# Performance work log

Measured on AMD Instinct MI355X. Metric: run time of the kernel, lower is better.

## Reference

```python
import jax, jax.numpy as jnp
import numpy as np

TEMPERATURE = 0.07
EPS = 1e-8
B, D, C = 4096, 512, 10


def setup_inputs() -> dict:
    key = jax.random.key(0)
    k1, k2 = jax.random.split(key)
    features = jax.random.normal(k1, (B, D), dtype=jnp.float32)
    cls = jax.random.randint(k2, (B,), 0, C)
    labels = jax.nn.one_hot(cls, C, dtype=jnp.float32)  # [B, C] one-hot
    return {"features": features, "labels": labels}


def reference(features, labels):
    b = features.shape[0]
    # L2-normalize rows
    feats = features / jnp.linalg.norm(features, axis=1, keepdims=True)
    sim = jnp.clip(feats @ feats.T / TEMPERATURE, -20.0, 20.0)  # [B, B]
    eye = jnp.eye(b, dtype=bool)
    sim = jnp.where(eye, -jnp.inf, sim)  # mask self-similarity

    labels_norm = labels / (labels.sum(axis=1, keepdims=True) + EPS)
    label_sim = labels_norm @ labels_norm.T  # [B, B]
    label_sim = jnp.where(eye, 0.0, label_sim)
    pos_mask = label_sim > 0.1  # [B, B] bool

    exp_sim = jnp.exp(sim)  # diag -> exp(-inf) = 0
    pos_sum = jnp.sum(jnp.where(pos_mask, exp_sim, 0.0), axis=1)  # [B]
    all_sum = jnp.sum(exp_sim, axis=1)  # diag already zero => off-diagonal sum
    loss_i = -jnp.log(pos_sum / (all_sum + EPS) + EPS)  # [B]

    valid = jnp.any(pos_mask, axis=1)  # rows with >=1 positive
    n_valid = jnp.sum(valid.astype(jnp.float32))
    total = jnp.sum(jnp.where(valid, loss_i, 0.0))
    return jnp.where(n_valid > 0, total / n_valid, 0.0)
```

## Files before the change

### kernel.cpp

```cpp
#include <hip/hip_runtime.h>


#define B_ROWS 4096
#define D_DIM  512
#define C_CLS  10
#define NT     64
#define NTILES (NT * (NT + 1) / 2)

typedef float f32x4 __attribute__((ext_vector_type(4)));

__device__ __forceinline__ void load_lds16(const void* g, void* l) {
  __builtin_amdgcn_global_load_lds(
      (const __attribute__((address_space(1))) unsigned int*)g,
      (__attribute__((address_space(3))) unsigned int*)l, 16, 0, 0);
}

__global__ __launch_bounds__(256) void prep_kernel(
    const float* __restrict__ feats, const float* __restrict__ labels,
    unsigned char* __restrict__ F8, int* __restrict__ cls,
    float* __restrict__ totals) {
  const int w = threadIdx.x >> 6, lane = threadIdx.x & 63;
  const int row = blockIdx.x * 4 + w;
  const float* fr = feats + (size_t)row * D_DIM;
  float4 v0 = ((const float4*)fr)[2 * lane];
  float4 v1 = ((const float4*)fr)[2 * lane + 1];
  float ss = v0.x*v0.x + v0.y*v0.y + v0.z*v0.z + v0.w*v0.w
           + v1.x*v1.x + v1.y*v1.y + v1.z*v1.z + v1.w*v1.w;
  #pragma unroll
  for (int m = 1; m < 64; m <<= 1) ss += __shfl_xor(ss, m, 64);
  float inv = 1.0f / sqrtf(ss);

  int p0 = __builtin_amdgcn_cvt_pk_fp8_f32(v0.x * inv, v0.y * inv, 0, 0);
  p0     = __builtin_amdgcn_cvt_pk_fp8_f32(v0.z * inv, v0.w * inv, p0, 1);
  int p1 = __builtin_amdgcn_cvt_pk_fp8_f32(v1.x * inv, v1.y * inv, 0, 0);
  p1     = __builtin_amdgcn_cvt_pk_fp8_f32(v1.z * inv, v1.w * inv, p1, 1);
  int2 pk; pk.x = p0; pk.y = p1;
  *(int2*)(F8 + (size_t)row * D_DIM + 8 * lane) = pk;

  float lv = (lane < C_CLS) ? labels[(size_t)row * C_CLS + lane] : 0.f;
  unsigned long long m = __ballot(lv > 0.5f);
  if (lane == 0) cls[row] = (int)(__ffsll((long long)m) - 1);
  if (blockIdx.x == 0 && threadIdx.x == 0) { totals[0] = 0.f; totals[1] = 0.f; }
}

__global__ __launch_bounds__(128) void sim_kernel(
    const unsigned char* __restrict__ F8, const int* __restrict__ cls,
    float* __restrict__ P_all, float* __restrict__ P_pos) {
  __shared__ __align__(16) unsigned char Abuf[64 * 128];
  __shared__ __align__(16) unsigned char Bbuf[64 * 128];
  __shared__ int clsA[64], clsB[64];
  __shared__ float g_row_all[64], g_row_pos[64];
  __shared__ float g_col_all[64], g_col_pos[64];

  int rem = blockIdx.x, bi = 0, rowlen = NT;
  while (rem >= rowlen) { rem -= rowlen; ++bi; --rowlen; }
  const int bj = bi + rem;
  const int i0 = bi * 64, j0 = bj * 64;
  const bool offdiag = (bi != bj);

  const int t = threadIdx.x;
  const int w = t >> 6;
  const int lane = t & 63;
  const int q = lane >> 4;
  const int cl = lane & 15;

  if (t < 64) { clsA[t] = cls[i0 + t]; g_col_all[t] = 0.f; g_col_pos[t] = 0.f; }
  else        clsB[t - 64] = cls[j0 + t - 64];

  f32x4 acc[2][4];
  #pragma unroll
  for (int ri = 0; ri < 2; ++ri)
    #pragma unroll
    for (int c = 0; c < 4; ++c) acc[ri][c] = (f32x4){0.f, 0.f, 0.f, 0.f};

  const int srow = lane >> 3;
  const int sg   = (lane & 7) ^ srow;

  for (int k0 = 0; k0 < D_DIM; k0 += 128) {
    __syncthreads();
    #pragma unroll
    for (int r = 0; r < 4; ++r) {
      const int rowbase = 32 * w + r * 8;
      load_lds16(F8 + (size_t)(i0 + rowbase + srow) * D_DIM + k0 + sg * 16,
                 &Abuf[rowbase * 128]);
      load_lds16(F8 + (size_t)(j0 + rowbase + srow) * D_DIM + k0 + sg * 16,
                 &Bbuf[rowbase * 128]);
    }
    __syncthreads();

    #pragma unroll
    for (int ks = 0; ks < 4; ++ks) {
      const int g = ks * 2 + (q >> 1);
      const int h = (q & 1) * 8;
      long af[2]; long bf[4];
      #pragma unroll
      for (int ri = 0; ri < 2; ++ri) {
        const int row = 32 * w + 16 * ri + cl;
        af[ri] = *(const long*)&Abuf[row * 128 + ((g ^ (row & 7)) * 16) + h];
      }
      #pragma unroll
      for (int c = 0; c < 4; ++c) {
        const int row = 16 * c + cl;
        bf[c] = *(const long*)&Bbuf[row * 128 + ((g ^ (row & 7)) * 16) + h];
      }
      #pragma unroll
      for (int ri = 0; ri < 2; ++ri)
        #pragma unroll
        for (int c = 0; c < 4; ++c)
          acc[ri][c] = __builtin_amdgcn_mfma_f32_16x16x32_fp8_fp8(
              af[ri], bf[c], acc[ri][c], 0, 0, 0);
    }
  }

  const float invT = 1.0f / 0.07f;
  float cs_all[4] = {0.f, 0.f, 0.f, 0.f};
  float cs_pos[4] = {0.f, 0.f, 0.f, 0.f};

  #pragma unroll
  for (int ri = 0; ri < 2; ++ri) {
    float sum_all[4] = {0.f, 0.f, 0.f, 0.f};
    float sum_pos[4] = {0.f, 0.f, 0.f, 0.f};
    #pragma unroll
    for (int c = 0; c < 4; ++c) {
      const int jloc = 16*c + cl;
      const int gj = j0 + jloc;
      const int cj = clsB[jloc];
      #pragma unroll
      for (int r = 0; r < 4; ++r) {
        const int iloc = 32*w + 16*ri + q*4 + r;
        const int gi = i0 + iloc;
        float s = acc[ri][c][r] * invT;
        s = fminf(fmaxf(s, -20.f), 20.f);
        const bool diag = (gi == gj);
        float e = diag ? 0.f : __expf(s);
        sum_all[r] += e;
        cs_all[c] += e;
        if (!diag && cj == clsA[iloc]) { sum_pos[r] += e; cs_pos[c] += e; }
      }
    }
    #pragma unroll
    for (int r = 0; r < 4; ++r) {
      float sa = sum_all[r], sp = sum_pos[r];
      #pragma unroll
      for (int m = 1; m < 16; m <<= 1) {
        sa += __shfl_xor(sa, m, 64);
        sp += __shfl_xor(sp, m, 64);
      }
      if (cl == 0) {
        const int rloc = 32*w + 16*ri + q*4 + r;
        g_row_all[rloc] = sa;
        g_row_pos[rloc] = sp;
      }
    }
  }

  if (offdiag) {
    #pragma unroll
    for (int c = 0; c < 4; ++c) {
      float sa = cs_all[c], sp = cs_pos[c];
      sa += __shfl_xor(sa, 16, 64); sa += __shfl_xor(sa, 32, 64);
      sp += __shfl_xor(sp, 16, 64); sp += __shfl_xor(sp, 32, 64);
      if (q == 0) {
        atomicAdd(&g_col_all[16*c + cl], sa);
        atomicAdd(&g_col_pos[16*c + cl], sp);
      }
    }
  }
  __syncthreads();

  if (w == 0) {
    const size_t base_row = ((size_t)bi * 64 + bj) * 64;
    P_all[base_row + lane] = g_row_all[lane];
    P_pos[base_row + lane] = g_row_pos[lane];
  } else if (offdiag) {
    const size_t base_col = ((size_t)bj * 64 + bi) * 64;
    P_all[base_col + lane] = g_col_all[lane];
    P_pos[base_col + lane] = g_col_pos[lane];
  }
}

__global__ __launch_bounds__(256) void finalize_kernel(
    const float* __restrict__ P_all, const float* __restrict__ P_pos,
    float* __restrict__ totals) {
  __shared__ float Sall[4096], Spos[4096];
  const int s = blockIdx.x;
  const int t = threadIdx.x;
  for (int i = t; i < 4096; i += 256) {
    Sall[i] = P_all[(size_t)s * 4096 + i];
    Spos[i] = P_pos[(size_t)s * 4096 + i];
  }
  __syncthreads();
  if (t < 64) {
    float a = 0.f, p = 0.f;
    #pragma unroll 8
    for (int k = 0; k < 64; ++k) {
      a += Sall[k * 64 + t];
      p += Spos[k * 64 + t];
    }
    float loss = 0.f, cnt = 0.f;
    if (p > 0.f) {
      loss = -logf(p / (a + 1e-8f) + 1e-8f);
      cnt = 1.f;
    }
    #pragma unroll
    for (int m = 1; m < 64; m <<= 1) {
      loss += __shfl_xor(loss, m, 64);
      cnt  += __shfl_xor(cnt, m, 64);
    }
    if (t == 0) {
      atomicAdd(&totals[0], loss);
      atomicAdd(&totals[1], cnt);
    }
  }
}

__global__ void div_kernel(const float* __restrict__ totals,
                           float* __restrict__ out) {
  out[0] = (totals[1] > 0.f) ? (totals[0] / totals[1]) : 0.f;
}

extern "C" void kernel_launch(void* const* d_in, const int* in_sizes, int n_in,
                              void* d_out, int out_size, void* d_ws, size_t ws_size,
                              hipStream_t stream) {
  const float* features = (const float*)d_in[0];
  const float* labels   = (const float*)d_in[1];
  float* out = (float*)d_out;

  unsigned char* F8     = (unsigned char*)d_ws;
  int*    cls    = (int*)((char*)d_ws + (size_t)B_ROWS * D_DIM);
  float*  P_all  = (float*)((char*)cls + B_ROWS * sizeof(int));
  float*  P_pos  = P_all + (size_t)NT * NT * 64;
  float*  totals = P_pos + (size_t)NT * NT * 64;

  prep_kernel<<<B_ROWS / 4, 256, 0, stream>>>(features, labels, F8, cls, totals);
  sim_kernel<<<NTILES, 128, 0, stream>>>(F8, cls, P_all, P_pos);
  finalize_kernel<<<NT, 256, 0, stream>>>(P_all, P_pos, totals);
  div_kernel<<<1, 1, 0, stream>>>(totals, out);
}
```

Baseline: 84.84 us.

## Load full-K tiles into LDS once and skip B load on diagonal tiles

Replaces the four-step K loop, which had two barriers per step, with a single bulk load of the whole 64x512 A and B tiles into LDS using a 32-way XOR swizzle, followed by 16 unrolled MFMA steps. On diagonal tiles the B load is skipped and A is reused. This drops the per-step barrier stalls but grows LDS to about 64KB per block, which lowers occupancy and removes any overlap between loads and compute.

```diff
diff --git a/kernel.cpp b/kernel.cpp
--- a/kernel.cpp
+++ b/kernel.cpp
@@ -46,8 +46,8 @@
 __global__ __launch_bounds__(128) void sim_kernel(
     const unsigned char* __restrict__ F8, const int* __restrict__ cls,
     float* __restrict__ P_all, float* __restrict__ P_pos) {
-  __shared__ __align__(16) unsigned char Abuf[64 * 128];
-  __shared__ __align__(16) unsigned char Bbuf[64 * 128];
+  __shared__ __align__(16) unsigned char Abuf[64 * 512];
+  __shared__ __align__(16) unsigned char Bbuf[64 * 512];
   __shared__ int clsA[64], clsB[64];
   __shared__ float g_row_all[64], g_row_pos[64];
   __shared__ float g_col_all[64], g_col_pos[64];
@@ -67,49 +67,54 @@
   if (t < 64) { clsA[t] = cls[i0 + t]; g_col_all[t] = 0.f; g_col_pos[t] = 0.f; }
   else        clsB[t - 64] = cls[j0 + t - 64];
 
+  {
+    const int s2 = lane >> 5;
+    const int cL = lane & 31;
+    const int base = (w == 0) ? i0 : j0;
+    unsigned char* buf = (w == 0) ? Abuf : Bbuf;
+    if (w == 0 || offdiag) {
+      #pragma unroll
+      for (int r = 0; r < 32; ++r) {
+        const int row = 2 * r + s2;
+        const int gc  = cL ^ (row & 31);
+        load_lds16(F8 + (size_t)(base + row) * D_DIM + gc * 16,
+                   &buf[(2 * r) * 512]);
+      }
+    }
+  }
+  __syncthreads();
+
+  const unsigned char* Bp = offdiag ? Bbuf : Abuf;
+
   f32x4 acc[2][4];
   #pragma unroll
   for (int ri = 0; ri < 2; ++ri)
     #pragma unroll
     for (int c = 0; c < 4; ++c) acc[ri][c] = (f32x4){0.f, 0.f, 0.f, 0.f};
 
-  const int srow = lane >> 3;
-  const int sg   = (lane & 7) ^ srow;
-
-  for (int k0 = 0; k0 < D_DIM; k0 += 128) {
-    __syncthreads();
-    #pragma unroll
-    for (int r = 0; r < 4; ++r) {
-      const int rowbase = 32 * w + r * 8;
-      load_lds16(F8 + (size_t)(i0 + rowbase + srow) * D_DIM + k0 + sg * 16,
-                 &Abuf[rowbase * 128]);
-      load_lds16(F8 + (size_t)(j0 + rowbase + srow) * D_DIM + k0 + sg * 16,
-                 &Bbuf[rowbase * 128]);
-    }
-    __syncthreads();
-
-    #pragma unroll
-    for (int ks = 0; ks < 4; ++ks) {
-      const int g = ks * 2 + (q >> 1);
-      const int h = (q & 1) * 8;
-      long af[2]; long bf[4];
-      #pragma unroll
-      for (int ri = 0; ri < 2; ++ri) {
-        const int row = 32 * w + 16 * ri + cl;
-        af[ri] = *(const long*)&Abuf[row * 128 + ((g ^ (row & 7)) * 16) + h];
-      }
-      #pragma unroll
-      for (int c = 0; c < 4; ++c) {
-        const int row = 16 * c + cl;
-        bf[c] = *(const long*)&Bbuf[row * 128 + ((g ^ (row & 7)) * 16) + h];
-      }
-      #pragma unroll
-      for (int ri = 0; ri < 2; ++ri)
-        #pragma unroll
-        for (int c = 0; c < 4; ++c)
-          acc[ri][c] = __builtin_amdgcn_mfma_f32_16x16x32_fp8_fp8(
-              af[ri], bf[c], acc[ri][c], 0, 0, 0);
-    }
+  const int h = (q & 1) * 8;
+  int arow[2], brow[4];
+  #pragma unroll
+  for (int ri = 0; ri < 2; ++ri) arow[ri] = 32 * w + 16 * ri + cl;
+  #pragma unroll
+  for (int c = 0; c < 4; ++c)    brow[c] = 16 * c + cl;
+
+  #pragma unroll
+  for (int ks = 0; ks < 16; ++ks) {
+    const int g = 2 * ks + (q >> 1);
+    long af[2]; long bf[4];
+    #pragma unroll
+    for (int ri = 0; ri < 2; ++ri)
+      af[ri] = *(const long*)&Abuf[arow[ri] * 512 + ((g ^ (arow[ri] & 31)) * 16) + h];
+    #pragma unroll
+    for (int c = 0; c < 4; ++c)
+      bf[c] = *(const long*)&Bp[brow[c] * 512 + ((g ^ (brow[c] & 31)) * 16) + h];
+    #pragma unroll
+    for (int ri = 0; ri < 2; ++ri)
+      #pragma unroll
+      for (int c = 0; c < 4; ++c)
+        acc[ri][c] = __builtin_amdgcn_mfma_f32_16x16x32_fp8_fp8(
+            af[ri], bf[c], acc[ri][c], 0, 0, 0);
   }
 
   const float invT = 1.0f / 0.07f;
```

Result: slower. 103.5 us (+22.0%).
